# Performance work log

Hardware: AMD Instinct MI355X
Metric: run time of the kernel (lower is better)

## Reference

```python
import jax, jax.numpy as jnp
import numpy as np


def gcn_conv(x, W, b, src, dst, dinv_sqrt, n_nodes):
    # PyG GCNConv: h = X W; out_i = sum_j norm_ij * h_j + b, norm = d_i^-1/2 d_j^-1/2
    h = x @ W  # [N, out]
    norm = dinv_sqrt[src] * dinv_sqrt[dst]  # [E]
    msg = h[src] * norm[:, None]  # [E, out]
    out = jax.ops.segment_sum(msg, dst, num_segments=n_nodes)
    return out + b


def setup_inputs() -> dict:
    key = jax.random.key(0)
    ks = jax.random.split(key, 12)
    N, E, G = 50000, 400000, 512
    x = jax.random.normal(ks[0], (N, 3), dtype=jnp.float32)
    edge_index = jax.random.randint(ks[1], (2, E), 0, N, dtype=jnp.int64)
    batch = jnp.sort(jax.random.randint(ks[2], (N,), 0, G, dtype=jnp.int64))
    def lin(k, fin, fout):
        kw, kb = jax.random.split(k)
        s = 1.0 / np.sqrt(fin)
        return (jax.random.uniform(kw, (fin, fout), jnp.float32, -s, s),
                jax.random.uniform(kb, (fout,), jnp.float32, -s, s))
    W1, b1 = lin(ks[3], 3, 100)
    W2, b2 = lin(ks[4], 100, 200)
    W3, b3 = lin(ks[5], 200, 100)
    W4, b4 = lin(ks[6], 100, 1)
    return {"x": x, "edge_index": edge_index, "batch": batch, "num_graphs": G,
            "W1": W1, "b1": b1, "W2": W2, "b2": b2,
            "W3": W3, "b3": b3, "W4": W4, "b4": b4}


def reference(x, edge_index, batch, num_graphs, W1, b1, W2, b2, W3, b3, W4, b4):
    N = x.shape[0]
    loop = jnp.arange(N, dtype=edge_index.dtype)
    src = jnp.concatenate([edge_index[0], loop])  # self-loops added (GCNConv default)
    dst = jnp.concatenate([edge_index[1], loop])
    deg = jax.ops.segment_sum(jnp.ones_like(src, dtype=x.dtype), dst, num_segments=N)
    dinv_sqrt = deg ** -0.5  # deg >= 1 due to self-loops

    h = jax.nn.silu(gcn_conv(x, W1, b1, src, dst, dinv_sqrt, N))
    h = jax.nn.silu(gcn_conv(h, W2, b2, src, dst, dinv_sqrt, N))

    # global_mean_pool over `batch` segments
    sums = jax.ops.segment_sum(h, batch, num_segments=num_graphs)  # [G, 200]
    cnts = jax.ops.segment_sum(jnp.ones((N,), h.dtype), batch, num_segments=num_graphs)
    pooled = sums / jnp.maximum(cnts, 1.0)[:, None]

    h = jax.nn.silu(pooled @ W3 + b3)
    out = h @ W4 + b4  # [G, 1]
    return out.squeeze(-1)
```

## Files before the change

### kernel.cpp

```cpp
#include <hip/hip_runtime.h>
#include <math.h>

#define WF 64

__device__ __forceinline__ float silu_f(float v){ return v / (1.0f + expf(-v)); }

__global__ __launch_bounds__(256) void k_count(const int* __restrict__ dst, int* __restrict__ cnt, int E){
  int e = blockIdx.x*blockDim.x + threadIdx.x;
  if (e < E) atomicAdd(&cnt[dst[e]], 1);
}

__global__ __launch_bounds__(256) void k_scan1(const int* __restrict__ cnt, int* __restrict__ rowstart, int* __restrict__ bsum, int N){
  __shared__ int s[256];
  int tid = threadIdx.x;
  int base = blockIdx.x*2048 + tid*8;
  int loc[8]; int tsum = 0;
#pragma unroll
  for (int j=0;j<8;++j){ int idx=base+j; int v = (idx<N)?cnt[idx]:0; loc[j]=tsum; tsum+=v; }
  s[tid]=tsum; __syncthreads();
  for (int off=1; off<256; off<<=1){
    int v = (tid>=off)? s[tid-off] : 0;
    __syncthreads();
    s[tid] += v;
    __syncthreads();
  }
  int texc = s[tid] - tsum;
  if (tid==255) bsum[blockIdx.x] = s[255];
#pragma unroll
  for (int j=0;j<8;++j){ int idx=base+j; if (idx<N) rowstart[idx] = texc + loc[j]; }
}

__global__ __launch_bounds__(256) void k_scan3(const int* __restrict__ bsum, const int* __restrict__ cnt,
                        const float* __restrict__ x,
                        int* __restrict__ rowstart, int* __restrict__ cursor,
                        float* __restrict__ dinv, float4* __restrict__ dxp,
                        int N, int E, int nb){
  __shared__ int boffs;
  int tid = threadIdx.x;
  int b = (blockIdx.x*blockDim.x) >> 11;
  if (tid < WF){
    int v = (tid < nb && tid < b) ? bsum[tid] : 0;
#pragma unroll
    for (int off=32; off; off>>=1) v += __shfl_down(v, off);
    if (tid==0) boffs = v;
  }
  __syncthreads();
  int idx = blockIdx.x*blockDim.x + tid;
  if (idx < N){
    int v = rowstart[idx] + boffs;
    rowstart[idx]=v; cursor[idx]=v;
    float di = rsqrtf((float)(cnt[idx]+1));
    dinv[idx] = di;
    float4 o;
    o.x = di;
    o.y = di*x[3*idx+0];
    o.z = di*x[3*idx+1];
    o.w = di*x[3*idx+2];
    dxp[idx] = o;
  }
  if (idx==0) rowstart[N]=E;
}

__global__ __launch_bounds__(256) void k_fill(const int* __restrict__ src, const int* __restrict__ dst,
                       int* __restrict__ cursor, int* __restrict__ colsrc, int E){
  int e = blockIdx.x*blockDim.x + threadIdx.x;
  if (e < E){
    int d = dst[e];
    int pos = atomicAdd(&cursor[d], 1);
    colsrc[pos] = src[e];
  }
}

__global__ __launch_bounds__(256) void k_l1(const float4* __restrict__ dxp,
                     const int* __restrict__ rowstart, const int* __restrict__ colsrc,
                     const float* __restrict__ W1, const float* __restrict__ b1,
                     float* __restrict__ h1s, int N){
  __shared__ float w[300];
  __shared__ float bb[100];
  int tid = threadIdx.x;
  for (int t=tid; t<300; t+=blockDim.x) w[t]=W1[t];
  for (int t=tid; t<100; t+=blockDim.x) bb[t]=b1[t];
  __syncthreads();
  int i = blockIdx.x*blockDim.x + tid;
  if (i >= N) return;
  float4 self = dxp[i];
  float di = self.x;
  float sx = self.y, sy = self.z, sz = self.w;
  int jb = rowstart[i], je = rowstart[i+1];
  int j = jb;
  for (; j+3 < je; j += 4){
    float4 r0 = dxp[colsrc[j]];
    float4 r1 = dxp[colsrc[j+1]];
    float4 r2 = dxp[colsrc[j+2]];
    float4 r3 = dxp[colsrc[j+3]];
    sx += (r0.y + r1.y) + (r2.y + r3.y);
    sy += (r0.z + r1.z) + (r2.z + r3.z);
    sz += (r0.w + r1.w) + (r2.w + r3.w);
  }
  for (; j < je; ++j){
    float4 r = dxp[colsrc[j]];
    sx += r.y; sy += r.z; sz += r.w;
  }
  sx*=di; sy*=di; sz*=di;
  float* orow = h1s + (size_t)i*100;
#pragma unroll
  for (int f0=0; f0<100; f0+=4){
    float4 o;
    o.x = silu_f(sx*w[f0+0] + sy*w[100+f0+0] + sz*w[200+f0+0] + bb[f0+0]);
    o.y = silu_f(sx*w[f0+1] + sy*w[100+f0+1] + sz*w[200+f0+1] + bb[f0+1]);
    o.z = silu_f(sx*w[f0+2] + sy*w[100+f0+2] + sz*w[200+f0+2] + bb[f0+2]);
    o.w = silu_f(sx*w[f0+3] + sy*w[100+f0+3] + sz*w[200+f0+3] + bb[f0+3]);
    *(float4*)&orow[f0] = o;
  }
}

__global__ __launch_bounds__(256) void k_agg2(const float* __restrict__ h1s, const int* __restrict__ rowstart,
                       const int* __restrict__ colsrc, const float* __restrict__ dinv,
                       float* __restrict__ a2, int N){
  int node = blockIdx.x*8 + (threadIdx.x >> 5);
  int lane = threadIdx.x & 31;
  if (node >= N) return;
  bool act = lane < 25;
  float di = dinv[node];
  float4 acc = make_float4(0.f,0.f,0.f,0.f);
  if (act){
    float4 v = *(const float4*)(h1s + (size_t)node*100 + lane*4);
    acc.x = di*v.x; acc.y = di*v.y; acc.z = di*v.z; acc.w = di*v.w;
  }
  int jb = rowstart[node], je = rowstart[node+1];
  int j = jb;
  for (; j+1 < je; j += 2){
    int u0 = colsrc[j];   float w0 = dinv[u0];
    int u1 = colsrc[j+1]; float w1 = dinv[u1];
    if (act){
      float4 r0 = *(const float4*)(h1s + (size_t)u0*100 + lane*4);
      float4 r1 = *(const float4*)(h1s + (size_t)u1*100 + lane*4);
      acc.x += w0*r0.x + w1*r1.x;
      acc.y += w0*r0.y + w1*r1.y;
      acc.z += w0*r0.z + w1*r1.z;
      acc.w += w0*r0.w + w1*r1.w;
    }
  }
  if (j < je){
    int u = colsrc[j]; float wv = dinv[u];
    if (act){
      float4 r = *(const float4*)(h1s + (size_t)u*100 + lane*4);
      acc.x += wv*r.x; acc.y += wv*r.y; acc.z += wv*r.z; acc.w += wv*r.w;
    }
  }
  if (act){
    float4 o;
    o.x = di*acc.x; o.y = di*acc.y; o.z = di*acc.z; o.w = di*acc.w;
    *(float4*)(a2 + (size_t)node*100 + lane*4) = o;
  }
}

#define CH 20
__global__ __launch_bounds__(256) void k_mm2(const float* __restrict__ a2, const float* __restrict__ W2,
                      const float* __restrict__ b2, const int* __restrict__ batch,
                      float* __restrict__ pooled, int N){
  __shared__ float aS[CH][132];
  __shared__ float wS[CH][48];
  int tid = threadIdx.x;
  int fg = tid & 3;
  int ng = tid >> 2;
  int fb = blockIdx.x;
  int n0 = blockIdx.y * 128;

  float acc[2][10];
#pragma unroll
  for (int i=0;i<2;++i)
#pragma unroll
    for (int j=0;j<10;++j) acc[i][j]=0.f;

  for (int kc = 0; kc < 5; ++kc){
    int kt = kc*CH;
    __syncthreads();
    for (int idx = tid; idx < 640; idx += 256){
      int n = idx / 5, q = idx - n*5;
      int gn = n0 + n;
      float4 v = make_float4(0.f,0.f,0.f,0.f);
      if (gn < N) v = *(const float4*)(a2 + (size_t)gn*100 + kt + q*4);
      aS[q*4+0][n] = v.x;
      aS[q*4+1][n] = v.y;
      aS[q*4+2][n] = v.z;
      aS[q*4+3][n] = v.w;
    }
    for (int idx = tid; idx < 800; idx += 256){
      int kl = idx / 40, f = idx - kl*40;
      int g = f / 10, j = f - g*10;
      wS[kl][g*12 + j] = W2[(size_t)(kt+kl)*200 + fb*40 + f];
    }
    __syncthreads();
#pragma unroll
    for (int kl = 0; kl < CH; ++kl){
      float a[2], w[10];
      *(float2*)a = *(const float2*)&aS[kl][ng*2];
      const float* wr = &wS[kl][fg*12];
      *(float4*)&w[0] = *(const float4*)&wr[0];
      *(float4*)&w[4] = *(const float4*)&wr[4];
      *(float2*)&w[8] = *(const float2*)&wr[8];
#pragma unroll
      for (int j=0;j<10;++j){
        float wv = w[j];
        acc[0][j] += a[0]*wv;
        acc[1][j] += a[1]*wv;
      }
    }
  }

  float* plL = &aS[0][0];
  __syncthreads();
  for (int idx = tid; idx < 320; idx += 256) plL[idx] = 0.f;
  __syncthreads();

  int fbase = fb*40 + fg*10;
  float bias[10];
#pragma unroll
  for (int j=0;j<10;++j) bias[j] = b2[fbase+j];
  int g0 = batch[n0];
  float s[10];
  int gprev = -1;
#pragma unroll
  for (int i=0;i<2;++i){
    int n = n0 + ng*2 + i;
    if (n < N){
      int g = batch[n];
      if (g != gprev){
        if (gprev >= 0){
          int dg = gprev - g0;
          if (dg < 8){
#pragma unroll
            for (int j=0;j<10;++j) atomicAdd(&plL[dg*40 + fg*10 + j], s[j]);
          } else {
#pragma unroll
            for (int j=0;j<10;++j) atomicAdd(&pooled[(size_t)gprev*200 + fbase + j], s[j]);
          }
        }
        gprev = g;
#pragma unroll
        for (int j=0;j<10;++j) s[j] = 0.f;
      }
#pragma unroll
      for (int j=0;j<10;++j) s[j] += silu_f(acc[i][j] + bias[j]);
    }
  }
  if (gprev >= 0){
    int dg = gprev - g0;
    if (dg < 8){
#pragma unroll
      for (int j=0;j<10;++j) atomicAdd(&plL[dg*40 + fg*10 + j], s[j]);
    } else {
#pragma unroll
      for (int j=0;j<10;++j) atomicAdd(&pooled[(size_t)gprev*200 + fbase + j], s[j]);
    }
  }
  __syncthreads();
  for (int idx = tid; idx < 320; idx += 256){
    float v = plL[idx];
    if (v != 0.f){
      int r = idx / 40, f = idx - r*40;
      atomicAdd(&pooled[(size_t)(g0+r)*200 + fb*40 + f], v);
    }
  }
}

__global__ __launch_bounds__(256) void k_head(const float* __restrict__ pooled, const int* __restrict__ batch,
                       const float* __restrict__ W3, const float* __restrict__ b3,
                       const float* __restrict__ W4, const float* __restrict__ b4,
                       float* __restrict__ out, int N){
  __shared__ float pl[200];
  __shared__ float h3[100];
  int g = blockIdx.x; int tid = threadIdx.x;
  int lo=0, hi=N;
  while (lo<hi){ int m=(lo+hi)>>1; if (batch[m] < g) lo=m+1; else hi=m; }
  int s = lo;
  hi=N;
  while (lo<hi){ int m=(lo+hi)>>1; if (batch[m] < g+1) lo=m+1; else hi=m; }
  int e = lo;
  float inv = (e>s) ? 1.0f/(float)(e-s) : 0.0f;
  if (tid < 200) pl[tid] = pooled[(size_t)g*200 + tid] * inv;
  __syncthreads();
  if (tid < 100){
    float acc = b3[tid];
    for (int k=0;k<200;++k) acc += pl[k]*W3[k*100+tid];
    h3[tid] = silu_f(acc);
  }
  __syncthreads();
  if (tid < WF){
    float p = 0.f;
    if (tid < 100)      p  = h3[tid]     * W4[tid];
    if (tid + 64 < 100) p += h3[tid+64]  * W4[tid+64];
#pragma unroll
    for (int off=32; off; off>>=1) p += __shfl_down(p, off);
    if (tid==0) out[g] = p + b4[0];
  }
}

extern "C" void kernel_launch(void* const* d_in, const int* in_sizes, int n_in,
                              void* d_out, int out_size, void* d_ws, size_t ws_size,
                              hipStream_t stream){
  const float* x  = (const float*)d_in[0];
  const int*   ei = (const int*)  d_in[1];
  const int* batch= (const int*)  d_in[2];
  const float* W1 = (const float*)d_in[4];
  const float* b1 = (const float*)d_in[5];
  const float* W2 = (const float*)d_in[6];
  const float* b2 = (const float*)d_in[7];
  const float* W3 = (const float*)d_in[8];
  const float* b3 = (const float*)d_in[9];
  const float* W4 = (const float*)d_in[10];
  const float* b4 = (const float*)d_in[11];
  float* out = (float*)d_out;

  int N = in_sizes[0]/3;
  int E = in_sizes[1]/2;
  int G = out_size;
  const int* src = ei;
  const int* dst = ei + E;

  char* base = (char*)d_ws; size_t off = 0;
  auto alloc = [&](size_t bytes)->void*{
    void* p = base + off;
    off = (off + bytes + 255) & ~(size_t)255;
    return p;
  };
  int*   cnt      = (int*)  alloc((size_t)N*4);
  float* pooled   = (float*)alloc((size_t)G*200*4);
  size_t zbytes   = off;
  int*   rowstart = (int*)  alloc((size_t)(N+1)*4);
  int*   cursor   = (int*)  alloc((size_t)N*4);
  int*   bsum     = (int*)  alloc(4096);
  int*   colsrc   = (int*)  alloc((size_t)E*4);
  float* dinv     = (float*)alloc((size_t)N*4);
  float4* dxp     = (float4*)alloc((size_t)N*16);
  float* h1s      = (float*)alloc((size_t)N*100*4);
  float* a2       = (float*)alloc((size_t)N*100*4);
  (void)ws_size; (void)n_in;

  hipMemsetAsync(base, 0, zbytes, stream);
  int gE = (E+255)/256;
  k_count<<<gE,256,0,stream>>>(dst, cnt, E);
  int nb = (N+2047)/2048;
  k_scan1<<<nb,256,0,stream>>>(cnt, rowstart, bsum, N);
  k_scan3<<<(N+255)/256,256,0,stream>>>(bsum, cnt, x, rowstart, cursor, dinv, dxp, N, E, nb);
  k_fill<<<gE,256,0,stream>>>(src, dst, cursor, colsrc, E);
  k_l1<<<(N+255)/256,256,0,stream>>>(dxp, rowstart, colsrc, W1, b1, h1s, N);
  k_agg2<<<(N+7)/8,256,0,stream>>>(h1s, rowstart, colsrc, dinv, a2, N);
  dim3 gmm(5, (N+127)/128);
  k_mm2<<<gmm,256,0,stream>>>(a2, W2, b2, batch, pooled, N);
  k_head<<<G,256,0,stream>>>(pooled, batch, W3, b3, W4, b4, out, N);
}
```

Before: 199.7 us.

## Enlarge k_mm2 per-thread register tile to 8x10 with 128-thread blocks

Restructures the second-layer matmul+pool kernel so each block covers 256 nodes with 128 threads, and each thread accumulates an 8-node by 10-feature tile instead of 2x10. The goal is more FMAs per shared-memory load of W2 and fewer blocks reloading W2. The A-tile staging now has each thread load whole-row float4s, which are strided rather than contiguous across lanes. Each thread's nodes are now 32 apart, so graph-boundary runs are shorter and pooling atomics may increase. The grid shrinks to about 980 small blocks and register pressure rises, which can lower occupancy.

```diff
diff --git a/kernel.cpp b/kernel.cpp
--- a/kernel.cpp
+++ b/kernel.cpp
@@ -156,37 +156,47 @@
 }
 
 #define CH 20
-__global__ __launch_bounds__(256) void k_mm2(const float* __restrict__ a2, const float* __restrict__ W2,
+__global__ __launch_bounds__(128) void k_mm2(const float* __restrict__ a2, const float* __restrict__ W2,
                       const float* __restrict__ b2, const int* __restrict__ batch,
                       float* __restrict__ pooled, int N){
-  __shared__ float aS[CH][132];
+  __shared__ float aS[CH][260];
   __shared__ float wS[CH][48];
   int tid = threadIdx.x;
   int fg = tid & 3;
   int ng = tid >> 2;
   int fb = blockIdx.x;
-  int n0 = blockIdx.y * 128;
-
-  float acc[2][10];
-#pragma unroll
-  for (int i=0;i<2;++i)
+  int n0 = blockIdx.y * 256;
+
+  int gn0 = n0 + tid, gn1 = n0 + tid + 128;
+  bool inb0 = (gn0 < N), inb1 = (gn1 < N);
+  const float* arow0 = a2 + (size_t)gn0*100;
+  const float* arow1 = a2 + (size_t)gn1*100;
+
+  float acc[8][10];
+#pragma unroll
+  for (int i=0;i<8;++i)
 #pragma unroll
     for (int j=0;j<10;++j) acc[i][j]=0.f;
 
   for (int kc = 0; kc < 5; ++kc){
     int kt = kc*CH;
     __syncthreads();
-    for (int idx = tid; idx < 640; idx += 256){
-      int n = idx / 5, q = idx - n*5;
-      int gn = n0 + n;
-      float4 v = make_float4(0.f,0.f,0.f,0.f);
-      if (gn < N) v = *(const float4*)(a2 + (size_t)gn*100 + kt + q*4);
-      aS[q*4+0][n] = v.x;
-      aS[q*4+1][n] = v.y;
-      aS[q*4+2][n] = v.z;
-      aS[q*4+3][n] = v.w;
-    }
-    for (int idx = tid; idx < 800; idx += 256){
+#pragma unroll
+    for (int c = 0; c < 5; ++c){
+      float4 v0 = make_float4(0.f,0.f,0.f,0.f);
+      float4 v1 = make_float4(0.f,0.f,0.f,0.f);
+      if (inb0) v0 = *(const float4*)(arow0 + kt + c*4);
+      if (inb1) v1 = *(const float4*)(arow1 + kt + c*4);
+      aS[c*4+0][tid] = v0.x;
+      aS[c*4+1][tid] = v0.y;
+      aS[c*4+2][tid] = v0.z;
+      aS[c*4+3][tid] = v0.w;
+      aS[c*4+0][tid+128] = v1.x;
+      aS[c*4+1][tid+128] = v1.y;
+      aS[c*4+2][tid+128] = v1.z;
+      aS[c*4+3][tid+128] = v1.w;
+    }
+    for (int idx = tid; idx < 800; idx += 128){
       int kl = idx / 40, f = idx - kl*40;
       int g = f / 10, j = f - g*10;
       wS[kl][g*12 + j] = W2[(size_t)(kt+kl)*200 + fb*40 + f];
@@ -194,24 +204,26 @@
     __syncthreads();
 #pragma unroll
     for (int kl = 0; kl < CH; ++kl){
-      float a[2], w[10];
-      *(float2*)a = *(const float2*)&aS[kl][ng*2];
+      float w[10];
       const float* wr = &wS[kl][fg*12];
       *(float4*)&w[0] = *(const float4*)&wr[0];
       *(float4*)&w[4] = *(const float4*)&wr[4];
       *(float2*)&w[8] = *(const float2*)&wr[8];
+      float a[8];
+#pragma unroll
+      for (int i=0;i<8;++i) a[i] = aS[kl][ng + 32*i];
 #pragma unroll
       for (int j=0;j<10;++j){
         float wv = w[j];
-        acc[0][j] += a[0]*wv;
-        acc[1][j] += a[1]*wv;
+#pragma unroll
+        for (int i=0;i<8;++i) acc[i][j] += a[i]*wv;
       }
     }
   }
 
   float* plL = &aS[0][0];
   __syncthreads();
-  for (int idx = tid; idx < 320; idx += 256) plL[idx] = 0.f;
+  for (int idx = tid; idx < 320; idx += 128) plL[idx] = 0.f;
   __syncthreads();
 
   int fbase = fb*40 + fg*10;
@@ -222,8 +234,8 @@
   float s[10];
   int gprev = -1;
 #pragma unroll
-  for (int i=0;i<2;++i){
-    int n = n0 + ng*2 + i;
+  for (int i=0;i<8;++i){
+    int n = n0 + ng + 32*i;
     if (n < N){
       int g = batch[n];
       if (g != gprev){
@@ -256,7 +268,7 @@
     }
   }
   __syncthreads();
-  for (int idx = tid; idx < 320; idx += 256){
+  for (int idx = tid; idx < 320; idx += 128){
     float v = plL[idx];
     if (v != 0.f){
       int r = idx / 40, f = idx - r*40;
@@ -347,7 +359,7 @@
   k_fill<<<gE,256,0,stream>>>(src, dst, cursor, colsrc, E);
   k_l1<<<(N+255)/256,256,0,stream>>>(dxp, rowstart, colsrc, W1, b1, h1s, N);
   k_agg2<<<(N+7)/8,256,0,stream>>>(h1s, rowstart, colsrc, dinv, a2, N);
-  dim3 gmm(5, (N+127)/128);
-  k_mm2<<<gmm,256,0,stream>>>(a2, W2, b2, batch, pooled, N);
+  dim3 gmm(5, (N+255)/256);
+  k_mm2<<<gmm,128,0,stream>>>(a2, W2, b2, batch, pooled, N);
   k_head<<<G,256,0,stream>>>(pooled, batch, W3, b3, W4, b4, out, N);
 }
```

Result: slower. 228.9 us (+14.6%).

## Use split-bf16 MFMA for the second-layer matmul in k_mm2

Applied to the files above, without the earlier changes.

Rewrites the fused matmul+SiLU+pool kernel to use 16x16x32 bf16 MFMA instructions. Each fp32 operand is split into high and low bf16 parts and combined with three MFMAs to approximate fp32 accuracy. The tiling changes to 64 nodes by 32 features per block, with the whole K=100 (padded to 128) staged in LDS at once. This aims to replace the scalar FMA inner loop with matrix-core throughput, at the cost of conversion work, padded feature tiles (7x32 for 200 features) and slightly reduced precision.

```diff
diff --git a/kernel.cpp b/kernel.cpp
--- a/kernel.cpp
+++ b/kernel.cpp
@@ -4,6 +4,9 @@
 #define WF 64
 
 __device__ __forceinline__ float silu_f(float v){ return v / (1.0f + expf(-v)); }
+
+typedef __attribute__((ext_vector_type(8))) short bf16x8;
+typedef __attribute__((ext_vector_type(4))) float f32x4;
 
 __global__ __launch_bounds__(256) void k_count(const int* __restrict__ dst, int* __restrict__ cnt, int E){
   int e = blockIdx.x*blockDim.x + threadIdx.x;
@@ -155,112 +158,116 @@
   }
 }
 
-#define CH 20
+#define AST 136
 __global__ __launch_bounds__(256) void k_mm2(const float* __restrict__ a2, const float* __restrict__ W2,
                       const float* __restrict__ b2, const int* __restrict__ batch,
                       float* __restrict__ pooled, int N){
-  __shared__ float aS[CH][132];
-  __shared__ float wS[CH][48];
+  __shared__ unsigned short aH[64*AST];
+  __shared__ unsigned short aL[64*AST];
+  __shared__ unsigned short wH[32*AST];
+  __shared__ unsigned short wL[32*AST];
   int tid = threadIdx.x;
-  int fg = tid & 3;
-  int ng = tid >> 2;
-  int fb = blockIdx.x;
-  int n0 = blockIdx.y * 128;
-
-  float acc[2][10];
-#pragma unroll
-  for (int i=0;i<2;++i)
-#pragma unroll
-    for (int j=0;j<10;++j) acc[i][j]=0.f;
-
-  for (int kc = 0; kc < 5; ++kc){
-    int kt = kc*CH;
-    __syncthreads();
-    for (int idx = tid; idx < 640; idx += 256){
-      int n = idx / 5, q = idx - n*5;
-      int gn = n0 + n;
-      float4 v = make_float4(0.f,0.f,0.f,0.f);
-      if (gn < N) v = *(const float4*)(a2 + (size_t)gn*100 + kt + q*4);
-      aS[q*4+0][n] = v.x;
-      aS[q*4+1][n] = v.y;
-      aS[q*4+2][n] = v.z;
-      aS[q*4+3][n] = v.w;
-    }
-    for (int idx = tid; idx < 800; idx += 256){
-      int kl = idx / 40, f = idx - kl*40;
-      int g = f / 10, j = f - g*10;
-      wS[kl][g*12 + j] = W2[(size_t)(kt+kl)*200 + fb*40 + f];
-    }
-    __syncthreads();
-#pragma unroll
-    for (int kl = 0; kl < CH; ++kl){
-      float a[2], w[10];
-      *(float2*)a = *(const float2*)&aS[kl][ng*2];
-      const float* wr = &wS[kl][fg*12];
-      *(float4*)&w[0] = *(const float4*)&wr[0];
-      *(float4*)&w[4] = *(const float4*)&wr[4];
-      *(float2*)&w[8] = *(const float2*)&wr[8];
-#pragma unroll
-      for (int j=0;j<10;++j){
-        float wv = w[j];
-        acc[0][j] += a[0]*wv;
-        acc[1][j] += a[1]*wv;
+  int l = tid & 63, w = tid >> 6;
+  int n0 = blockIdx.x * 64;
+  int fb = blockIdx.y;
+
+  for (int idx = tid; idx < 4096; idx += 256){
+    int f = idx & 31, k = idx >> 5;
+    int gf = fb*32 + f;
+    float v = (k < 100 && gf < 200) ? W2[(size_t)k*200 + gf] : 0.f;
+    unsigned int b = __float_as_uint(v);
+    unsigned int h = (b + 0x8000u) >> 16;
+    float hf = __uint_as_float(h << 16);
+    float lo = v - hf;
+    unsigned int bl = __float_as_uint(lo);
+    unsigned int hl = (bl + 0x8000u) >> 16;
+    wH[f*AST + k] = (unsigned short)h;
+    wL[f*AST + k] = (unsigned short)hl;
+  }
+  for (int idx = tid; idx < 8192; idx += 256){
+    int n = idx >> 7, k = idx & 127;
+    int gn = n0 + n;
+    float v = (k < 100 && gn < N) ? a2[(size_t)gn*100 + k] : 0.f;
+    unsigned int b = __float_as_uint(v);
+    unsigned int h = (b + 0x8000u) >> 16;
+    float hf = __uint_as_float(h << 16);
+    float lo = v - hf;
+    unsigned int bl = __float_as_uint(lo);
+    unsigned int hl = (bl + 0x8000u) >> 16;
+    aH[n*AST + k] = (unsigned short)h;
+    aL[n*AST + k] = (unsigned short)hl;
+  }
+  __syncthreads();
+
+  f32x4 acc0 = {0.f,0.f,0.f,0.f};
+  f32x4 acc1 = {0.f,0.f,0.f,0.f};
+  int row = l & 15;
+  int kg  = l >> 4;
+#pragma unroll
+  for (int ks = 0; ks < 4; ++ks){
+    int ko = ks*32 + kg*8;
+    int ao  = (w*16 + row)*AST + ko;
+    bf16x8 ah = *(const bf16x8*)&aH[ao];
+    bf16x8 al = *(const bf16x8*)&aL[ao];
+    int wo0 = row*AST + ko;
+    int wo1 = (16 + row)*AST + ko;
+    bf16x8 wh0 = *(const bf16x8*)&wH[wo0];
+    bf16x8 wl0 = *(const bf16x8*)&wL[wo0];
+    bf16x8 wh1 = *(const bf16x8*)&wH[wo1];
+    bf16x8 wl1 = *(const bf16x8*)&wL[wo1];
+    acc0 = __builtin_amdgcn_mfma_f32_16x16x32_bf16(ah, wh0, acc0, 0, 0, 0);
+    acc0 = __builtin_amdgcn_mfma_f32_16x16x32_bf16(ah, wl0, acc0, 0, 0, 0);
+    acc0 = __builtin_amdgcn_mfma_f32_16x16x32_bf16(al, wh0, acc0, 0, 0, 0);
+    acc1 = __builtin_amdgcn_mfma_f32_16x16x32_bf16(ah, wh1, acc1, 0, 0, 0);
+    acc1 = __builtin_amdgcn_mfma_f32_16x16x32_bf16(ah, wl1, acc1, 0, 0, 0);
+    acc1 = __builtin_amdgcn_mfma_f32_16x16x32_bf16(al, wh1, acc1, 0, 0, 0);
+  }
+
+  float* plL = (float*)aH;
+  __syncthreads();
+  if (tid < 256) plL[tid] = 0.f;
+  __syncthreads();
+
+  int g0 = batch[n0];
+#pragma unroll
+  for (int ft = 0; ft < 2; ++ft){
+    f32x4 a = ft ? acc1 : acc0;
+    int fl = ft*16 + row;
+    int gf = fb*32 + fl;
+    if (gf < 200){
+      float bias = b2[gf];
+      float s = 0.f;
+      int gprev = -1;
+#pragma unroll
+      for (int r = 0; r < 4; ++r){
+        int node = n0 + w*16 + kg*4 + r;
+        if (node < N){
+          int g = batch[node];
+          if (g != gprev){
+            if (gprev >= 0){
+              int dg = gprev - g0;
+              if (dg < 8) atomicAdd(&plL[dg*32 + fl], s);
+              else        atomicAdd(&pooled[(size_t)gprev*200 + gf], s);
+            }
+            gprev = g; s = 0.f;
+          }
+          s += silu_f(a[r] + bias);
+        }
+      }
+      if (gprev >= 0){
+        int dg = gprev - g0;
+        if (dg < 8) atomicAdd(&plL[dg*32 + fl], s);
+        else        atomicAdd(&pooled[(size_t)gprev*200 + gf], s);
       }
     }
   }
-
-  float* plL = &aS[0][0];
-  __syncthreads();
-  for (int idx = tid; idx < 320; idx += 256) plL[idx] = 0.f;
-  __syncthreads();
-
-  int fbase = fb*40 + fg*10;
-  float bias[10];
-#pragma unroll
-  for (int j=0;j<10;++j) bias[j] = b2[fbase+j];
-  int g0 = batch[n0];
-  float s[10];
-  int gprev = -1;
-#pragma unroll
-  for (int i=0;i<2;++i){
-    int n = n0 + ng*2 + i;
-    if (n < N){
-      int g = batch[n];
-      if (g != gprev){
-        if (gprev >= 0){
-          int dg = gprev - g0;
-          if (dg < 8){
-#pragma unroll
-            for (int j=0;j<10;++j) atomicAdd(&plL[dg*40 + fg*10 + j], s[j]);
-          } else {
-#pragma unroll
-            for (int j=0;j<10;++j) atomicAdd(&pooled[(size_t)gprev*200 + fbase + j], s[j]);
-          }
-        }
-        gprev = g;
-#pragma unroll
-        for (int j=0;j<10;++j) s[j] = 0.f;
-      }
-#pragma unroll
-      for (int j=0;j<10;++j) s[j] += silu_f(acc[i][j] + bias[j]);
-    }
-  }
-  if (gprev >= 0){
-    int dg = gprev - g0;
-    if (dg < 8){
-#pragma unroll
-      for (int j=0;j<10;++j) atomicAdd(&plL[dg*40 + fg*10 + j], s[j]);
-    } else {
-#pragma unroll
-      for (int j=0;j<10;++j) atomicAdd(&pooled[(size_t)gprev*200 + fbase + j], s[j]);
-    }
-  }
-  __syncthreads();
-  for (int idx = tid; idx < 320; idx += 256){
-    float v = plL[idx];
+  __syncthreads();
+  if (tid < 256){
+    float v = plL[tid];
     if (v != 0.f){
-      int r = idx / 40, f = idx - r*40;
-      atomicAdd(&pooled[(size_t)(g0+r)*200 + fb*40 + f], v);
+      int r = tid >> 5, f = tid & 31;
+      int gf = fb*32 + f;
+      if (gf < 200) atomicAdd(&pooled[(size_t)(g0+r)*200 + gf], v);
     }
   }
 }
@@ -347,7 +354,7 @@
   k_fill<<<gE,256,0,stream>>>(src, dst, cursor, colsrc, E);
   k_l1<<<(N+255)/256,256,0,stream>>>(dxp, rowstart, colsrc, W1, b1, h1s, N);
   k_agg2<<<(N+7)/8,256,0,stream>>>(h1s, rowstart, colsrc, dinv, a2, N);
-  dim3 gmm(5, (N+127)/128);
+  dim3 gmm((N+63)/64, 7);
   k_mm2<<<gmm,256,0,stream>>>(a2, W2, b2, batch, pooled, N);
   k_head<<<G,256,0,stream>>>(pooled, batch, W3, b3, W4, b4, out, N);
 }
```

Result: slower. 265.7 us (+33.0%).
